# Kernel optimization log

Measured on AMD Instinct MI355X. Metric: run time of the kernel, lower is better.

Reference implementation:

```python
import jax, jax.numpy as jnp
import numpy as np

H = 224  # config.output_height
W = 224  # config.output_width
N = 381  # config.num_frequency_bins (one splat per bin)
B = 16   # frames rendered per batch


def setup_inputs() -> dict:
    key = jax.random.key(0)
    k1, k2, k3 = jax.random.split(key, 3)
    # positions in [-0.9, 0.9] (spiral stays inside the frame)
    positions = jax.random.uniform(k1, (B, N, 2), dtype=jnp.float32, minval=-0.9, maxval=0.9)
    colors = jax.random.uniform(k2, (B, N, 3), dtype=jnp.float32)  # RGB in [0,1]
    # sizes in pixels, matching base_size=2 + size_scale=8*softplus(...)
    sizes = jax.random.uniform(k3, (B, N), dtype=jnp.float32, minval=2.0, maxval=10.0)
    return {"positions": positions, "colors": colors, "sizes": sizes}


def reference(positions, colors, sizes):
    """Soft (differentiable) rasterization of Gaussian point splats.

    positions: [B,N,2] in [-1,1]; colors: [B,N,3] in [0,1]; sizes: [B,N] pixels.
    Returns image [B,H,W,3] in [0,1].
    """
    gy = jnp.linspace(-1.0, 1.0, H, dtype=positions.dtype)
    gx = jnp.linspace(-1.0, 1.0, W, dtype=positions.dtype)
    # squared distance from every pixel to every point: [B,N,H,W]
    dx = gx[None, None, None, :] - positions[:, :, 0, None, None]
    dy = gy[None, None, :, None] - positions[:, :, 1, None, None]
    d2 = dx * dx + dy * dy
    # pixel size -> normalized coords ([-1,1] spans H pixels)
    sigma = sizes * (2.0 / H)  # [B,N]
    inv_two_var = 1.0 / (2.0 * sigma * sigma + 1e-8)
    weights = jnp.exp(-d2 * inv_two_var[:, :, None, None])  # [B,N,H,W]
    image = jnp.einsum('bnhw,bnc->bhwc', weights, colors)   # accumulate splats
    return jnp.clip(image, 0.0, 1.0)
```

## Files before the change

### kernel.cpp

```cpp
#include <hip/hip_runtime.h>
#include <math.h>

#define HH 224
#define WW 224
#define NS 381
#define BB 16
#define TPB 256
#define TILE_W 32
#define TILE_H 32
#define TILES_X (WW / TILE_W)
#define BLKS_PER_IMG (TILES_X * (HH / TILE_H))
#define NBLK (BB * BLKS_PER_IMG)
#define NS_PAD 384
#define CUT 19.93f

__global__ __launch_bounds__(TPB) void splat_render(const float* __restrict__ pos,
                                                    const float* __restrict__ col,
                                                    const float* __restrict__ siz,
                                                    float* __restrict__ out) {
    __shared__ float4 geo[NS_PAD];
    __shared__ int cnt;

    int blk = blockIdx.x;
    int b = blk / BLKS_PER_IMG;
    int t = blk - b * BLKS_PER_IMG;
    int tile_y = t / TILES_X;
    int tile_x = t - tile_y * TILES_X;

    if (threadIdx.x == 0) cnt = 0;
    __syncthreads();

    const float gstep = 2.0f / (float)(WW - 1);
    float x0 = -1.0f + (float)(tile_x * TILE_W) * gstep;
    float x1 = x0 + (float)(TILE_W - 1) * gstep;
    float y0 = -1.0f + (float)(tile_y * TILE_H) * gstep;
    float y1 = y0 + (float)(TILE_H - 1) * gstep;

    const float2* pb = (const float2*)(pos + (size_t)b * NS * 2);
    const float*  cb = col + (size_t)b * NS * 3;
    const float*  sb = siz + (size_t)b * NS;
    int lane = threadIdx.x & 63;

    for (int r = 0; r < 2; ++r) {
        int i = threadIdx.x + r * TPB;
        bool pass = false;
        float4 A = make_float4(0.f, 0.f, 0.f, 0.f);
        if (i < NS) {
            float2 p = pb[i];
            float sg = sb[i] * (2.0f / (float)HH);
            float itv = 1.0f / (2.0f * sg * sg + 1e-8f);
            float ss = sqrtf(itv * 1.44269504088896340736f);
            float u = p.x * ss, v = p.y * ss;
            float dxm = fmaxf(fmaxf(x0 * ss - u, u - x1 * ss), 0.0f);
            float dym = fmaxf(fmaxf(y0 * ss - v, v - y1 * ss), 0.0f);
            pass = fmaf(dxm, dxm, dym * dym) < CUT;
            if (pass) {
                unsigned pr = (unsigned)fmaf(cb[3 * i + 0], 1023.0f, 0.5f);
                unsigned pg = (unsigned)fmaf(cb[3 * i + 1], 1023.0f, 0.5f);
                unsigned pc = (unsigned)fmaf(cb[3 * i + 2], 1023.0f, 0.5f);
                A = make_float4(ss, -u, -v, __uint_as_float(pr | (pg << 10) | (pc << 20)));
            }
        }
        unsigned long long mask = __ballot(pass);
        int ofs = __popcll(mask & ((1ull << lane) - 1ull));
        int tot = __popcll(mask);
        int base = 0;
        if (lane == 0 && tot) base = atomicAdd(&cnt, tot);
        base = __shfl(base, 0);
        if (pass) geo[base + ofs] = A;
    }
    __syncthreads();
    int m = cnt;
    int m4 = (m + 3) & ~3;
    if (threadIdx.x < (m4 - m))
        geo[m + threadIdx.x] = make_float4(0.f, 0.f, 1000.0f, 0.f);
    __syncthreads();
    m4 = __builtin_amdgcn_readfirstlane(m4);

    int tx = threadIdx.x & 7;
    int ty = threadIdx.x >> 3;
    int w0 = tile_x * TILE_W + tx * 4;
    int h  = tile_y * TILE_H + ty;
    float gy  = -1.0f + (float)h * gstep;
    float gx0 = -1.0f + (float)w0 * gstep;
    float gx1 = gx0 + gstep;
    float gx2 = gx0 + 2.0f * gstep;
    float gx3 = gx0 + 3.0f * gstep;

    float r0 = 0.f, g0 = 0.f, b0 = 0.f;
    float r1 = 0.f, g1 = 0.f, b1 = 0.f;
    float r2 = 0.f, g2 = 0.f, b2 = 0.f;
    float r3 = 0.f, g3 = 0.f, b3 = 0.f;

#pragma unroll 4
    for (int j = 0; j < m4; ++j) {
        float4 A = geo[j];
        float dy  = fmaf(gy, A.x, A.z);
        float ndd = -(dy * dy);
        if (ndd > -CUT) {
            unsigned pk = __float_as_uint(A.w);
            const float q = (1.0f / 1023.0f);
            float cr = (float)(pk & 1023u) * q;
            float cg = (float)((pk >> 10) & 1023u) * q;
            float cc = (float)(pk >> 20) * q;
            float dx0 = fmaf(gx0, A.x, A.y);
            float dx1 = fmaf(gx1, A.x, A.y);
            float dx2 = fmaf(gx2, A.x, A.y);
            float dx3 = fmaf(gx3, A.x, A.y);
            float we0 = __builtin_amdgcn_exp2f(fmaf(-dx0, dx0, ndd));
            float we1 = __builtin_amdgcn_exp2f(fmaf(-dx1, dx1, ndd));
            float we2 = __builtin_amdgcn_exp2f(fmaf(-dx2, dx2, ndd));
            float we3 = __builtin_amdgcn_exp2f(fmaf(-dx3, dx3, ndd));
            r0 = fmaf(we0, cr, r0); g0 = fmaf(we0, cg, g0); b0 = fmaf(we0, cc, b0);
            r1 = fmaf(we1, cr, r1); g1 = fmaf(we1, cg, g1); b1 = fmaf(we1, cc, b1);
            r2 = fmaf(we2, cr, r2); g2 = fmaf(we2, cg, g2); b2 = fmaf(we2, cc, b2);
            r3 = fmaf(we3, cr, r3); g3 = fmaf(we3, cg, g3); b3 = fmaf(we3, cc, b3);
        }
    }

    float4* o4 = (float4*)(out + ((size_t)b * (HH * WW) + (size_t)h * WW + w0) * 3);
    o4[0] = make_float4(fminf(r0, 1.f), fminf(g0, 1.f), fminf(b0, 1.f), fminf(r1, 1.f));
    o4[1] = make_float4(fminf(g1, 1.f), fminf(b1, 1.f), fminf(r2, 1.f), fminf(g2, 1.f));
    o4[2] = make_float4(fminf(b2, 1.f), fminf(r3, 1.f), fminf(g3, 1.f), fminf(b3, 1.f));
}

extern "C" void kernel_launch(void* const* d_in, const int* in_sizes, int n_in,
                              void* d_out, int out_size, void* d_ws, size_t ws_size,
                              hipStream_t stream) {
    const float* pos = (const float*)d_in[0];
    const float* col = (const float*)d_in[1];
    const float* siz = (const float*)d_in[2];
    float* out = (float*)d_out;
    splat_render<<<NBLK, TPB, 0, stream>>>(pos, col, siz, out);
}
```

Before: 77.70 us.

## Factor Gaussian splat into separable terms and accumulate with fp16 MFMA

Exploits the separability of the Gaussian, exp(-dx^2-dy^2) = exp(-dx^2)*exp(-dy^2). Per chunk of 32 splats, the block precomputes the x-factors and the color-weighted y-factors in shared memory as fp16. It then accumulates the tile image with 16x16x32 f16 MFMA instructions instead of per-pixel exp and FMA loops. This replaces the per-pixel transcendental work with a small GEMM, at the cost of extra barriers per chunk, a transposing epilogue through shared memory, and fp16 rounding of the weights.

```diff
diff --git a/kernel.cpp b/kernel.cpp
--- a/kernel.cpp
+++ b/kernel.cpp
@@ -13,6 +13,24 @@
 #define NBLK (BB * BLKS_PER_IMG)
 #define NS_PAD 384
 #define CUT 19.93f
+#define CH 32
+#define EY_STRIDE 33
+#define EXT_STRIDE 40
+#define MT_STRIDE 40
+#define OUT_STRIDE 97
+
+typedef _Float16 f16x8 __attribute__((ext_vector_type(8)));
+typedef _Float16 f16x2 __attribute__((ext_vector_type(2)));
+typedef float    f32x4 __attribute__((ext_vector_type(4)));
+
+union SharedU {
+    struct {
+        float    ey[CH * EY_STRIDE];
+        _Float16 ext[TILE_W * EXT_STRIDE];
+        _Float16 mt[96 * MT_STRIDE];
+    } s;
+    float outb[TILE_W * OUT_STRIDE];
+};
 
 __global__ __launch_bounds__(TPB) void splat_render(const float* __restrict__ pos,
                                                     const float* __restrict__ col,
@@ -20,6 +38,7 @@
                                                     float* __restrict__ out) {
     __shared__ float4 geo[NS_PAD];
     __shared__ int cnt;
+    __shared__ SharedU u;
 
     int blk = blockIdx.x;
     int b = blk / BLKS_PER_IMG;
@@ -40,6 +59,7 @@
     const float*  cb = col + (size_t)b * NS * 3;
     const float*  sb = siz + (size_t)b * NS;
     int lane = threadIdx.x & 63;
+    int wave = threadIdx.x >> 6;
 
     for (int r = 0; r < 2; ++r) {
         int i = threadIdx.x + r * TPB;
@@ -50,15 +70,15 @@
             float sg = sb[i] * (2.0f / (float)HH);
             float itv = 1.0f / (2.0f * sg * sg + 1e-8f);
             float ss = sqrtf(itv * 1.44269504088896340736f);
-            float u = p.x * ss, v = p.y * ss;
-            float dxm = fmaxf(fmaxf(x0 * ss - u, u - x1 * ss), 0.0f);
-            float dym = fmaxf(fmaxf(y0 * ss - v, v - y1 * ss), 0.0f);
+            float u_ = p.x * ss, v_ = p.y * ss;
+            float dxm = fmaxf(fmaxf(x0 * ss - u_, u_ - x1 * ss), 0.0f);
+            float dym = fmaxf(fmaxf(y0 * ss - v_, v_ - y1 * ss), 0.0f);
             pass = fmaf(dxm, dxm, dym * dym) < CUT;
             if (pass) {
                 unsigned pr = (unsigned)fmaf(cb[3 * i + 0], 1023.0f, 0.5f);
                 unsigned pg = (unsigned)fmaf(cb[3 * i + 1], 1023.0f, 0.5f);
                 unsigned pc = (unsigned)fmaf(cb[3 * i + 2], 1023.0f, 0.5f);
-                A = make_float4(ss, -u, -v, __uint_as_float(pr | (pg << 10) | (pc << 20)));
+                A = make_float4(ss, -u_, -v_, __uint_as_float(pr | (pg << 10) | (pc << 20)));
             }
         }
         unsigned long long mask = __ballot(pass);
@@ -71,57 +91,96 @@
     }
     __syncthreads();
     int m = cnt;
-    int m4 = (m + 3) & ~3;
-    if (threadIdx.x < (m4 - m))
-        geo[m + threadIdx.x] = make_float4(0.f, 0.f, 1000.0f, 0.f);
+    int m_pad = (m + (CH - 1)) & ~(CH - 1);
+    for (int i = m + threadIdx.x; i < m_pad; i += TPB)
+        geo[i] = make_float4(0.f, 0.f, 0.f, 0.f);
     __syncthreads();
-    m4 = __builtin_amdgcn_readfirstlane(m4);
+
+    int ct = wave & 1;
+    int qbase = (wave >> 1) * 48;
+    f32x4 acc0 = {0.f, 0.f, 0.f, 0.f};
+    f32x4 acc1 = {0.f, 0.f, 0.f, 0.f};
+    f32x4 acc2 = {0.f, 0.f, 0.f, 0.f};
+
+    int p2  = threadIdx.x & 15;
+    int rEy = threadIdx.x & 31;
+    float gyr = y0 + (float)rEy * gstep;
+
+    for (int nb = 0; nb < m_pad; nb += CH) {
+#pragma unroll
+        for (int k = 0; k < 4; ++k) {
+            int n = (threadIdx.x >> 5) + 8 * k;
+            float4 A = geo[nb + n];
+            float dy = fmaf(gyr, A.x, A.z);
+            u.s.ey[n * EY_STRIDE + rEy] = __builtin_amdgcn_exp2f(-dy * dy);
+        }
+        __syncthreads();
+        float4 A0 = geo[nb + 2 * p2];
+        float4 A1 = geo[nb + 2 * p2 + 1];
+#pragma unroll
+        for (int k = 0; k < 2; ++k) {
+            int c = (threadIdx.x >> 4) + 16 * k;
+            float gxc = x0 + (float)c * gstep;
+            float dx0 = fmaf(gxc, A0.x, A0.y);
+            float dx1 = fmaf(gxc, A1.x, A1.y);
+            f16x2 h;
+            h.x = (_Float16)__builtin_amdgcn_exp2f(-dx0 * dx0);
+            h.y = (_Float16)__builtin_amdgcn_exp2f(-dx1 * dx1);
+            *(f16x2*)&u.s.ext[c * EXT_STRIDE + 2 * p2] = h;
+        }
+        unsigned pk0 = __float_as_uint(A0.w), pk1 = __float_as_uint(A1.w);
+#pragma unroll
+        for (int k = 0; k < 6; ++k) {
+            int q = (threadIdx.x >> 4) + 16 * k;
+            int r = (q * 21846) >> 16;
+            int chn = q - 3 * r;
+            float cf0 = (float)((pk0 >> (10 * chn)) & 1023u) * (1.0f / 1023.0f);
+            float cf1 = (float)((pk1 >> (10 * chn)) & 1023u) * (1.0f / 1023.0f);
+            f16x2 h;
+            h.x = (_Float16)(u.s.ey[(2 * p2) * EY_STRIDE + r] * cf0);
+            h.y = (_Float16)(u.s.ey[(2 * p2 + 1) * EY_STRIDE + r] * cf1);
+            *(f16x2*)&u.s.mt[q * MT_STRIDE + 2 * p2] = h;
+        }
+        __syncthreads();
+        {
+            int koff = (lane >> 4) * 8;
+            f16x8 a  = *(const f16x8*)&u.s.ext[((lane & 15) + 16 * ct) * EXT_STRIDE + koff];
+            f16x8 b0 = *(const f16x8*)&u.s.mt[(qbase +  0 + (lane & 15)) * MT_STRIDE + koff];
+            f16x8 b1 = *(const f16x8*)&u.s.mt[(qbase + 16 + (lane & 15)) * MT_STRIDE + koff];
+            f16x8 b2 = *(const f16x8*)&u.s.mt[(qbase + 32 + (lane & 15)) * MT_STRIDE + koff];
+            acc0 = __builtin_amdgcn_mfma_f32_16x16x32_f16(a, b0, acc0, 0, 0, 0);
+            acc1 = __builtin_amdgcn_mfma_f32_16x16x32_f16(a, b1, acc1, 0, 0, 0);
+            acc2 = __builtin_amdgcn_mfma_f32_16x16x32_f16(a, b2, acc2, 0, 0, 0);
+        }
+        __syncthreads();
+    }
+
+    int drow = ct * 16 + (lane >> 4) * 4;
+    int dcol = qbase + (lane & 15);
+#pragma unroll
+    for (int rr = 0; rr < 4; ++rr) {
+        u.outb[(drow + rr) * OUT_STRIDE + dcol +  0] = acc0[rr];
+        u.outb[(drow + rr) * OUT_STRIDE + dcol + 16] = acc1[rr];
+        u.outb[(drow + rr) * OUT_STRIDE + dcol + 32] = acc2[rr];
+    }
+    __syncthreads();
 
     int tx = threadIdx.x & 7;
     int ty = threadIdx.x >> 3;
     int w0 = tile_x * TILE_W + tx * 4;
     int h  = tile_y * TILE_H + ty;
-    float gy  = -1.0f + (float)h * gstep;
-    float gx0 = -1.0f + (float)w0 * gstep;
-    float gx1 = gx0 + gstep;
-    float gx2 = gx0 + 2.0f * gstep;
-    float gx3 = gx0 + 3.0f * gstep;
-
-    float r0 = 0.f, g0 = 0.f, b0 = 0.f;
-    float r1 = 0.f, g1 = 0.f, b1 = 0.f;
-    float r2 = 0.f, g2 = 0.f, b2 = 0.f;
-    float r3 = 0.f, g3 = 0.f, b3 = 0.f;
-
-#pragma unroll 4
-    for (int j = 0; j < m4; ++j) {
-        float4 A = geo[j];
-        float dy  = fmaf(gy, A.x, A.z);
-        float ndd = -(dy * dy);
-        if (ndd > -CUT) {
-            unsigned pk = __float_as_uint(A.w);
-            const float q = (1.0f / 1023.0f);
-            float cr = (float)(pk & 1023u) * q;
-            float cg = (float)((pk >> 10) & 1023u) * q;
-            float cc = (float)(pk >> 20) * q;
-            float dx0 = fmaf(gx0, A.x, A.y);
-            float dx1 = fmaf(gx1, A.x, A.y);
-            float dx2 = fmaf(gx2, A.x, A.y);
-            float dx3 = fmaf(gx3, A.x, A.y);
-            float we0 = __builtin_amdgcn_exp2f(fmaf(-dx0, dx0, ndd));
-            float we1 = __builtin_amdgcn_exp2f(fmaf(-dx1, dx1, ndd));
-            float we2 = __builtin_amdgcn_exp2f(fmaf(-dx2, dx2, ndd));
-            float we3 = __builtin_amdgcn_exp2f(fmaf(-dx3, dx3, ndd));
-            r0 = fmaf(we0, cr, r0); g0 = fmaf(we0, cg, g0); b0 = fmaf(we0, cc, b0);
-            r1 = fmaf(we1, cr, r1); g1 = fmaf(we1, cg, g1); b1 = fmaf(we1, cc, b1);
-            r2 = fmaf(we2, cr, r2); g2 = fmaf(we2, cg, g2); b2 = fmaf(we2, cc, b2);
-            r3 = fmaf(we3, cr, r3); g3 = fmaf(we3, cg, g3); b3 = fmaf(we3, cc, b3);
-        }
+    float v[12];
+#pragma unroll
+    for (int j = 0; j < 4; ++j) {
+        int c = tx * 4 + j;
+        v[3 * j + 0] = fminf(u.outb[c * OUT_STRIDE + 3 * ty + 0], 1.f);
+        v[3 * j + 1] = fminf(u.outb[c * OUT_STRIDE + 3 * ty + 1], 1.f);
+        v[3 * j + 2] = fminf(u.outb[c * OUT_STRIDE + 3 * ty + 2], 1.f);
     }
-
     float4* o4 = (float4*)(out + ((size_t)b * (HH * WW) + (size_t)h * WW + w0) * 3);
-    o4[0] = make_float4(fminf(r0, 1.f), fminf(g0, 1.f), fminf(b0, 1.f), fminf(r1, 1.f));
-    o4[1] = make_float4(fminf(g1, 1.f), fminf(b1, 1.f), fminf(r2, 1.f), fminf(g2, 1.f));
-    o4[2] = make_float4(fminf(b2, 1.f), fminf(r3, 1.f), fminf(g3, 1.f), fminf(b3, 1.f));
+    o4[0] = make_float4(v[0], v[1], v[2], v[3]);
+    o4[1] = make_float4(v[4], v[5], v[6], v[7]);
+    o4[2] = make_float4(v[8], v[9], v[10], v[11]);
 }
 
 extern "C" void kernel_launch(void* const* d_in, const int* in_sizes, int n_in,
```

Measured after the change: 67.91 us. 12.6% less time.
